# Optimization experiments

Measured on AMD Instinct MI355X. Metric: run time of the kernel, lower is better.

## Reference

```python
import jax, jax.numpy as jnp
import numpy as np

D_MODEL = 1024
NUM_HEADS = 16
D_K = D_MODEL // NUM_HEADS


def setup_inputs() -> dict:
    key = jax.random.key(0)
    ks = jax.random.split(key, 9)
    B, S = 4, 2048
    s = 1.0 / np.sqrt(D_MODEL)
    inp = {
        "x": jax.random.normal(ks[0], (B, S, D_MODEL), dtype=jnp.float32),
        "wq": jax.random.uniform(ks[1], (D_MODEL, D_MODEL), jnp.float32, -s, s),
        "bq": jax.random.uniform(ks[2], (D_MODEL,), jnp.float32, -s, s),
        "wk": jax.random.uniform(ks[3], (D_MODEL, D_MODEL), jnp.float32, -s, s),
        "bk": jax.random.uniform(ks[4], (D_MODEL,), jnp.float32, -s, s),
        "wv": jax.random.uniform(ks[5], (D_MODEL, D_MODEL), jnp.float32, -s, s),
        "bv": jax.random.uniform(ks[6], (D_MODEL,), jnp.float32, -s, s),
        "wo": jax.random.uniform(ks[7], (D_MODEL, D_MODEL), jnp.float32, -s, s),
        "bo": jax.random.uniform(ks[8], (D_MODEL,), jnp.float32, -s, s),
    }
    return inp


def reference(x, wq, bq, wk, bk, wv, bv, wo, bo):
    B, S, _ = x.shape
    H, Dk = NUM_HEADS, D_K
    # QKV projections; weights stored as (in, out) so y = x @ w + b
    q = (x @ wq + bq).reshape(B, S, H, Dk).transpose(0, 2, 1, 3)  # (B,H,S,Dk)
    k = (x @ wk + bk).reshape(B, S, H, Dk).transpose(0, 2, 1, 3)
    v = (x @ wv + bv).reshape(B, S, H, Dk).transpose(0, 2, 1, 3)
    scores = jnp.einsum("bhqd,bhkd->bhqk", q, k) / jnp.sqrt(jnp.float32(Dk))
    causal = jnp.tril(jnp.ones((S, S), dtype=bool))  # True = keep
    scores = jnp.where(causal, scores, jnp.float32(-jnp.inf))
    attn = jax.nn.softmax(scores, axis=-1)  # dropout=0 (eval)
    out = jnp.einsum("bhqk,bhkd->bhqd", attn, v)
    out = out.transpose(0, 2, 1, 3).reshape(B, S, H * Dk)
    return out @ wo + bo
```

## Files before the change

kernel.cpp:

```cpp
#include <hip/hip_runtime.h>
#include <hip/hip_bf16.h>


#define D_MODEL 1024
#define NHEADS  16
#define DK      64
#define BATCH   4
#define SEQ     2048
#define MROWS   (BATCH*SEQ)

typedef short bvec8 __attribute__((ext_vector_type(8)));
typedef float fvec4 __attribute__((ext_vector_type(4)));

__device__ __forceinline__ unsigned short f2bf(float f) {
    unsigned int x = __float_as_uint(f);
    x += 0x7fffu + ((x >> 16) & 1u);
    return (unsigned short)(x >> 16);
}

__device__ __forceinline__ unsigned pack_bf16x2(float a, float b) {
#if __has_builtin(__builtin_amdgcn_cvt_pk_bf16_f32)
    typedef __bf16 bf16x2_t __attribute__((ext_vector_type(2)));
    union { bf16x2_t v; unsigned u; } cv;
    cv.v = __builtin_amdgcn_cvt_pk_bf16_f32(a, b);
    return cv.u;
#else
    return (unsigned)f2bf(a) | ((unsigned)f2bf(b) << 16);
#endif
}

__device__ __forceinline__ float fast_exp2(float x) {
#if __has_builtin(__builtin_amdgcn_exp2f)
    return __builtin_amdgcn_exp2f(x);
#else
    return exp2f(x);
#endif
}


__global__ void f32_to_bf16_k(const float* __restrict__ in,
                              unsigned short* __restrict__ out, int n4) {
    int i = blockIdx.x * 256 + threadIdx.x;
    if (i < n4) {
        float4 v = ((const float4*)in)[i];
        ushort4 o;
        o.x = f2bf(v.x); o.y = f2bf(v.y); o.z = f2bf(v.z); o.w = f2bf(v.w);
        ((ushort4*)out)[i] = o;
    }
}

__global__ void transpose_to_bf16_k(const float* __restrict__ W,
                                    unsigned short* __restrict__ Wt) {
    __shared__ float tile[32][33];
    int n0 = blockIdx.x * 32, k0 = blockIdx.y * 32;
    int tx = threadIdx.x & 31;
    int ty = (threadIdx.x >> 5) * 4;
#pragma unroll
    for (int i = 0; i < 4; ++i)
        tile[ty + i][tx] = W[(k0 + ty + i) * D_MODEL + n0 + tx];
    __syncthreads();
#pragma unroll
    for (int i = 0; i < 4; ++i)
        Wt[(n0 + ty + i) * D_MODEL + k0 + tx] = f2bf(tile[tx][ty + i]);
}

__global__ void build_cbias_k(const float* __restrict__ bq, const float* __restrict__ bk,
                              const float* __restrict__ bv, float* __restrict__ cb) {
    int i = blockIdx.x * 256 + threadIdx.x;
    float v = (i < 1024) ? bq[i] : (i < 2048) ? bk[i - 1024] : bv[i - 2048];
    cb[i] = v;
}

__global__ __launch_bounds__(256, 4)
void gemm_glds(const unsigned short* __restrict__ A,
               const unsigned short* __restrict__ Bt,
               const float* __restrict__ bias,
               unsigned short* __restrict__ oq,
               unsigned short* __restrict__ ok,
               unsigned short* __restrict__ ov,
               float* __restrict__ of,
               float qscale, int mode) {
    __shared__ __align__(16) unsigned short As[128 * 64];
    __shared__ __align__(16) unsigned short Bs[128 * 64];

    const int tid  = threadIdx.x;
    const int lane = tid & 63;
    const int w    = tid >> 6;
    const int wr   = w >> 1, wc = w & 1;
    const int quad = lane >> 4, l16 = lane & 15;
    const int rowBlock = blockIdx.y * 128;
    const int colBlock = blockIdx.x * 128;

    const int lrow   = lane >> 3;
    const int gchunk = (lane & 7) ^ lrow;

    fvec4 acc[4][4] = {};

    for (int k0 = 0; k0 < D_MODEL; k0 += 64) {
        __syncthreads();
#pragma unroll
        for (int n = 0; n < 4; ++n) {
            const int g = w * 4 + n;
            const int ra = rowBlock + g * 8 + lrow;
            const int ca = colBlock + g * 8 + lrow;
            __builtin_amdgcn_global_load_lds(
                (const __attribute__((address_space(1))) void*)
                    &A[(size_t)ra * D_MODEL + k0 + gchunk * 8],
                (__attribute__((address_space(3))) void*)&As[g * 512], 16, 0, 0);
            __builtin_amdgcn_global_load_lds(
                (const __attribute__((address_space(1))) void*)
                    &Bt[(size_t)ca * D_MODEL + k0 + gchunk * 8],
                (__attribute__((address_space(3))) void*)&Bs[g * 512], 16, 0, 0);
        }
        __syncthreads();
#pragma unroll
        for (int kc = 0; kc < 2; ++kc) {
            bvec8 af[4], bfr[4];
#pragma unroll
            for (int i = 0; i < 4; ++i) {
                int r = wr * 64 + i * 16 + l16;
                af[i] = *(const bvec8*)&As[r * 64 + (((kc * 4 + quad) ^ (l16 & 7)) * 8)];
            }
#pragma unroll
            for (int j = 0; j < 4; ++j) {
                int r = wc * 64 + j * 16 + l16;
                bfr[j] = *(const bvec8*)&Bs[r * 64 + (((kc * 4 + quad) ^ (l16 & 7)) * 8)];
            }
#pragma unroll
            for (int i = 0; i < 4; ++i)
#pragma unroll
                for (int j = 0; j < 4; ++j)
                    acc[i][j] = __builtin_amdgcn_mfma_f32_16x16x32_bf16(
                        af[i], bfr[j], acc[i][j], 0, 0, 0);
        }
    }

    if (mode == 0) {
#pragma unroll
        for (int i = 0; i < 4; ++i) {
#pragma unroll
            for (int j = 0; j < 4; ++j) {
                int ncol = colBlock + wc * 64 + j * 16 + l16;
                int which = ncol >> 10;
                int nn = ncol & 1023;
                int h = nn >> 6, d = nn & 63;
                float bv = bias[ncol];
#pragma unroll
                for (int r = 0; r < 4; ++r) {
                    int mrow = rowBlock + wr * 64 + i * 16 + quad * 4 + r;
                    int b = mrow >> 11, s = mrow & (SEQ - 1);
                    float v = acc[i][j][r] + bv;
                    if (which == 0)
                        oq[(((b * NHEADS + h) * SEQ + s) * DK) + d] = f2bf(v * qscale);
                    else if (which == 1)
                        ok[(((b * NHEADS + h) * SEQ + s) * DK) + d] = f2bf(v);
                    else
                        ov[(((b * NHEADS + h) * DK + d) * SEQ) + s] = f2bf(v);
                }
            }
        }
    } else {
#pragma unroll
        for (int i = 0; i < 4; ++i) {
#pragma unroll
            for (int j = 0; j < 4; ++j) {
                int ncol = colBlock + wc * 64 + j * 16 + l16;
                float bv = bias[ncol];
#pragma unroll
                for (int r = 0; r < 4; ++r) {
                    int mrow = rowBlock + wr * 64 + i * 16 + quad * 4 + r;
                    of[(size_t)mrow * D_MODEL + ncol] = acc[i][j][r] + bv;
                }
            }
        }
    }
}

__global__ __launch_bounds__(256, 3)
void attn_mfma6(const unsigned short* __restrict__ Q,
                const unsigned short* __restrict__ K,
                const unsigned short* __restrict__ Vt,
                unsigned short* __restrict__ O) {
    __shared__ __align__(16) unsigned short Ksm[64 * 64];
    __shared__ __align__(16) unsigned short Vsm[64 * 64];
    __shared__ __align__(16) unsigned short Pl[4][32 * 64];

    const int tid  = threadIdx.x;
    const int lane = tid & 63;
    const int wq   = tid >> 6;
    const int quad = lane >> 4, l16 = lane & 15;
    const int bx = blockIdx.x;
    const int qt = (bx & 1) ? ((bx - 1) >> 1) : (15 - (bx >> 1));
    const int h = blockIdx.y, b = blockIdx.z;

    const size_t bhq = ((size_t)b * NHEADS + h) * SEQ * DK;
    const unsigned short* Qb = Q + bhq;
    const unsigned short* Kb = K + bhq;
    const unsigned short* Vb = Vt + bhq;

    const int q0 = qt * 128 + wq * 32;

    bvec8 qf[2][2];
#pragma unroll
    for (int qg = 0; qg < 2; ++qg)
#pragma unroll
        for (int kc = 0; kc < 2; ++kc)
            qf[qg][kc] = *(const bvec8*)&Qb[(q0 + qg * 16 + l16) * DK + kc * 32 + quad * 8];

    const int sr = tid >> 2;
    const int sc = tid & 3;
    const int sp0 = ((sc) ^ (sr & 7)) * 8;
    const int sp1 = ((sc + 4) ^ (sr & 7)) * 8;
    unsigned short* Pw = &Pl[wq][0];

    const int ktmax = 2 * qt + 1;
    const int ktact = 2 * qt + (wq >> 1);
    const int mofs  = (wq & 1) << 5;

    bvec8 kr0, kr1, vr0, vr1;
    {
        const unsigned short* kg = Kb + sr * DK;
        kr0 = *(const bvec8*)(kg + sc * 8);
        kr1 = *(const bvec8*)(kg + (sc + 4) * 8);
        const unsigned short* vg = Vb + sr * SEQ;
        vr0 = *(const bvec8*)(vg + sc * 8);
        vr1 = *(const bvec8*)(vg + (sc + 4) * 8);
    }

    fvec4 acc[2][4] = {};
    float lp[2] = {0.f, 0.f};

    for (int kt = 0; kt <= ktmax; ++kt) {
        *(bvec8*)&Ksm[sr * 64 + sp0] = kr0;
        *(bvec8*)&Ksm[sr * 64 + sp1] = kr1;
        *(bvec8*)&Vsm[sr * 64 + sp0] = vr0;
        *(bvec8*)&Vsm[sr * 64 + sp1] = vr1;
        __syncthreads();
        if (kt < ktmax) {
            const unsigned short* kg = Kb + ((kt + 1) * 64 + sr) * DK;
            kr0 = *(const bvec8*)(kg + sc * 8);
            kr1 = *(const bvec8*)(kg + (sc + 4) * 8);
            const unsigned short* vg = Vb + sr * SEQ + (kt + 1) * 64;
            vr0 = *(const bvec8*)(vg + sc * 8);
            vr1 = *(const bvec8*)(vg + (sc + 4) * 8);
        }
        if (kt <= ktact) {
#pragma unroll
            for (int t4 = 0; t4 < 4; ++t4) {
                fvec4 s[2] = {};
#pragma unroll
                for (int kc = 0; kc < 2; ++kc) {
                    bvec8 af = *(const bvec8*)
                        &Ksm[(t4 * 16 + l16) * 64 + (((kc * 4 + quad) ^ (l16 & 7)) * 8)];
#pragma unroll
                    for (int qg = 0; qg < 2; ++qg)
                        s[qg] = __builtin_amdgcn_mfma_f32_16x16x32_bf16(
                            af, qf[qg][kc], s[qg], 0, 0, 0);
                }
                if (kt == ktact) {
#pragma unroll
                    for (int qg = 0; qg < 2; ++qg)
#pragma unroll
                        for (int r = 0; r < 4; ++r) {
                            int key = t4 * 16 + quad * 4 + r - mofs;
                            int qq  = qg * 16 + l16;
                            if (key > qq) s[qg][r] = -__builtin_inff();
                        }
                }
#pragma unroll
                for (int qg = 0; qg < 2; ++qg) {
                    float p0 = fast_exp2(s[qg][0]);
                    float p1 = fast_exp2(s[qg][1]);
                    float p2 = fast_exp2(s[qg][2]);
                    float p3 = fast_exp2(s[qg][3]);
                    lp[qg] += (p0 + p1) + (p2 + p3);
                    uint2 pk;
                    pk.x = pack_bf16x2(p0, p1);
                    pk.y = pack_bf16x2(p2, p3);
                    *(uint2*)&Pw[(qg * 16 + l16) * 64 +
                                 (((t4 * 2 + (quad >> 1)) ^ (l16 & 7)) * 8) +
                                 (quad & 1) * 4] = pk;
                }
            }

#pragma unroll
            for (int kc = 0; kc < 2; ++kc) {
                bvec8 ap[2];
#pragma unroll
                for (int qg = 0; qg < 2; ++qg)
                    ap[qg] = *(const bvec8*)
                        &Pw[(qg * 16 + l16) * 64 + (((kc * 4 + quad) ^ (l16 & 7)) * 8)];
#pragma unroll
                for (int dt = 0; dt < 4; ++dt) {
                    bvec8 bv = *(const bvec8*)
                        &Vsm[(dt * 16 + l16) * 64 + (((kc * 4 + quad) ^ (l16 & 7)) * 8)];
#pragma unroll
                    for (int qg = 0; qg < 2; ++qg)
                        acc[qg][dt] = __builtin_amdgcn_mfma_f32_16x16x32_bf16(
                            ap[qg], bv, acc[qg][dt], 0, 0, 0);
                }
            }
        }
        __syncthreads();
    }

#pragma unroll
    for (int qg = 0; qg < 2; ++qg) {
        float lr = lp[qg];
        lr += __shfl_xor(lr, 16);
        lr += __shfl_xor(lr, 32);
        float invv[4];
#pragma unroll
        for (int r = 0; r < 4; ++r)
            invv[r] = 1.f / __shfl(lr, quad * 4 + r);
#pragma unroll
        for (int r = 0; r < 4; ++r) {
            size_t row = (size_t)(b * SEQ + q0 + qg * 16 + quad * 4 + r);
            unsigned short* dst = O + row * D_MODEL + h * DK + l16;
#pragma unroll
            for (int dt = 0; dt < 4; ++dt)
                dst[dt * 16] = f2bf(acc[qg][dt][r] * invv[r]);
        }
    }
}


extern "C" void kernel_launch(void* const* d_in, const int* in_sizes, int n_in,
                              void* d_out, int out_size, void* d_ws, size_t ws_size,
                              hipStream_t stream) {
    const float* x  = (const float*)d_in[0];
    const float* wq = (const float*)d_in[1];
    const float* bq = (const float*)d_in[2];
    const float* wk = (const float*)d_in[3];
    const float* bk = (const float*)d_in[4];
    const float* wv = (const float*)d_in[5];
    const float* bv = (const float*)d_in[6];
    const float* wo = (const float*)d_in[7];
    const float* bo = (const float*)d_in[8];
    float* out = (float*)d_out;

    char* ws = (char*)d_ws;
    const size_t MB = 1u << 20;
    unsigned short* xb    = (unsigned short*)(ws);
    unsigned short* wqkvt = (unsigned short*)(ws + 16 * MB);
    unsigned short* wot   = (unsigned short*)(ws + 22 * MB);
    unsigned short* qb    = (unsigned short*)(ws + 24 * MB);
    unsigned short* kb    = (unsigned short*)(ws + 40 * MB);
    unsigned short* vtb   = (unsigned short*)(ws + 56 * MB);
    unsigned short* ab    = (unsigned short*)(ws + 72 * MB);
    float* cbias = (float*)(ws + 72 * MB);

    f32_to_bf16_k<<<(MROWS * D_MODEL / 4 + 255) / 256, 256, 0, stream>>>(
        x, xb, MROWS * D_MODEL / 4);
    dim3 tg(32, 32);
    transpose_to_bf16_k<<<tg, 256, 0, stream>>>(wq, wqkvt);
    transpose_to_bf16_k<<<tg, 256, 0, stream>>>(wk, wqkvt + 1024 * 1024);
    transpose_to_bf16_k<<<tg, 256, 0, stream>>>(wv, wqkvt + 2 * 1024 * 1024);
    transpose_to_bf16_k<<<tg, 256, 0, stream>>>(wo, wot);
    build_cbias_k<<<12, 256, 0, stream>>>(bq, bk, bv, cbias);

    const float QSCALE = 0.125f * 1.44269504088896340736f;

    gemm_glds<<<dim3(3072 / 128, MROWS / 128), 256, 0, stream>>>(
        xb, wqkvt, cbias, qb, kb, vtb, nullptr, QSCALE, 0);

    attn_mfma6<<<dim3(SEQ / 128, NHEADS, BATCH), 256, 0, stream>>>(qb, kb, vtb, ab);

    gemm_glds<<<dim3(D_MODEL / 128, MROWS / 128), 256, 0, stream>>>(
        ab, wot, bo, nullptr, nullptr, nullptr, out, 1.0f, 1);
}
```

Measured before the change: 323.6 us.

## Double-buffer K/V tiles in attention, halve P scratch, merge weight transposes

The attention kernel now double-buffers the K and V shared-memory tiles. This removes the second barrier per key tile, since the next tile is written into the other buffer after compute. The P staging buffer is split into two 32-key halves interleaved with the PV MFMAs, which shrinks LDS use so launch bounds can target 4 blocks per CU. The four weight-transpose launches are merged into one kernel with a z grid dimension to cut launch overhead. The risk is higher register pressure at 4 waves per SIMD, plus the changed swizzle patterns.

After: 318.4 us. About the same (-1.6%).

```diff
diff --git a/kernel.cpp b/kernel.cpp
--- a/kernel.cpp
+++ b/kernel.cpp
@@ -49,9 +49,14 @@
     }
 }
 
-__global__ void transpose_to_bf16_k(const float* __restrict__ W,
-                                    unsigned short* __restrict__ Wt) {
+__global__ void transpose_all_k(const float* __restrict__ wq, const float* __restrict__ wk,
+                                const float* __restrict__ wv, const float* __restrict__ wo,
+                                unsigned short* __restrict__ wqkvt,
+                                unsigned short* __restrict__ wot) {
     __shared__ float tile[32][33];
+    const int z = blockIdx.z;
+    const float* W = (z == 0) ? wq : (z == 1) ? wk : (z == 2) ? wv : wo;
+    unsigned short* Wt = (z == 3) ? wot : wqkvt + (size_t)z * D_MODEL * D_MODEL;
     int n0 = blockIdx.x * 32, k0 = blockIdx.y * 32;
     int tx = threadIdx.x & 31;
     int ty = (threadIdx.x >> 5) * 4;
@@ -176,14 +181,14 @@
     }
 }
 
-__global__ __launch_bounds__(256, 3)
-void attn_mfma6(const unsigned short* __restrict__ Q,
+__global__ __launch_bounds__(256, 4)
+void attn_mfma7(const unsigned short* __restrict__ Q,
                 const unsigned short* __restrict__ K,
                 const unsigned short* __restrict__ Vt,
                 unsigned short* __restrict__ O) {
-    __shared__ __align__(16) unsigned short Ksm[64 * 64];
-    __shared__ __align__(16) unsigned short Vsm[64 * 64];
-    __shared__ __align__(16) unsigned short Pl[4][32 * 64];
+    __shared__ __align__(16) unsigned short Ksm[2][64 * 64];
+    __shared__ __align__(16) unsigned short Vsm[2][64 * 64];
+    __shared__ __align__(16) unsigned short Pl[4][32 * 32];
 
     const int tid  = threadIdx.x;
     const int lane = tid & 63;
@@ -225,17 +230,18 @@
         const unsigned short* vg = Vb + sr * SEQ;
         vr0 = *(const bvec8*)(vg + sc * 8);
         vr1 = *(const bvec8*)(vg + (sc + 4) * 8);
+        *(bvec8*)&Ksm[0][sr * 64 + sp0] = kr0;
+        *(bvec8*)&Ksm[0][sr * 64 + sp1] = kr1;
+        *(bvec8*)&Vsm[0][sr * 64 + sp0] = vr0;
+        *(bvec8*)&Vsm[0][sr * 64 + sp1] = vr1;
     }
 
     fvec4 acc[2][4] = {};
     float lp[2] = {0.f, 0.f};
 
     for (int kt = 0; kt <= ktmax; ++kt) {
-        *(bvec8*)&Ksm[sr * 64 + sp0] = kr0;
-        *(bvec8*)&Ksm[sr * 64 + sp1] = kr1;
-        *(bvec8*)&Vsm[sr * 64 + sp0] = vr0;
-        *(bvec8*)&Vsm[sr * 64 + sp1] = vr1;
         __syncthreads();
+        const int buf = kt & 1;
         if (kt < ktmax) {
             const unsigned short* kg = Kb + ((kt + 1) * 64 + sr) * DK;
             kr0 = *(const bvec8*)(kg + sc * 8);
@@ -245,55 +251,57 @@
             vr1 = *(const bvec8*)(vg + (sc + 4) * 8);
         }
         if (kt <= ktact) {
-#pragma unroll
-            for (int t4 = 0; t4 < 4; ++t4) {
-                fvec4 s[2] = {};
-#pragma unroll
-                for (int kc = 0; kc < 2; ++kc) {
-                    bvec8 af = *(const bvec8*)
-                        &Ksm[(t4 * 16 + l16) * 64 + (((kc * 4 + quad) ^ (l16 & 7)) * 8)];
-#pragma unroll
-                    for (int qg = 0; qg < 2; ++qg)
-                        s[qg] = __builtin_amdgcn_mfma_f32_16x16x32_bf16(
-                            af, qf[qg][kc], s[qg], 0, 0, 0);
+            const unsigned short* Kbuf = &Ksm[buf][0];
+            const unsigned short* Vbuf = &Vsm[buf][0];
+#pragma unroll
+            for (int half = 0; half < 2; ++half) {
+#pragma unroll
+                for (int tl = 0; tl < 2; ++tl) {
+                    const int t4 = half * 2 + tl;
+                    fvec4 s[2] = {};
+#pragma unroll
+                    for (int kc = 0; kc < 2; ++kc) {
+                        bvec8 af = *(const bvec8*)
+                            &Kbuf[(t4 * 16 + l16) * 64 + (((kc * 4 + quad) ^ (l16 & 7)) * 8)];
+#pragma unroll
+                        for (int qg = 0; qg < 2; ++qg)
+                            s[qg] = __builtin_amdgcn_mfma_f32_16x16x32_bf16(
+                                af, qf[qg][kc], s[qg], 0, 0, 0);
+                    }
+                    if (kt == ktact) {
+#pragma unroll
+                        for (int qg = 0; qg < 2; ++qg)
+#pragma unroll
+                            for (int r = 0; r < 4; ++r) {
+                                int key = t4 * 16 + quad * 4 + r - mofs;
+                                int qq  = qg * 16 + l16;
+                                if (key > qq) s[qg][r] = -__builtin_inff();
+                            }
+                    }
+#pragma unroll
+                    for (int qg = 0; qg < 2; ++qg) {
+                        float p0 = fast_exp2(s[qg][0]);
+                        float p1 = fast_exp2(s[qg][1]);
+                        float p2 = fast_exp2(s[qg][2]);
+                        float p3 = fast_exp2(s[qg][3]);
+                        lp[qg] += (p0 + p1) + (p2 + p3);
+                        uint2 pk;
+                        pk.x = pack_bf16x2(p0, p1);
+                        pk.y = pack_bf16x2(p2, p3);
+                        *(uint2*)&Pw[(qg * 16 + l16) * 32 +
+                                     (((tl * 2 + (quad >> 1)) ^ (l16 & 3)) * 8) +
+                                     (quad & 1) * 4] = pk;
+                    }
                 }
-                if (kt == ktact) {
-#pragma unroll
-                    for (int qg = 0; qg < 2; ++qg)
-#pragma unroll
-                        for (int r = 0; r < 4; ++r) {
-                            int key = t4 * 16 + quad * 4 + r - mofs;
-                            int qq  = qg * 16 + l16;
-                            if (key > qq) s[qg][r] = -__builtin_inff();
-                        }
-                }
-#pragma unroll
-                for (int qg = 0; qg < 2; ++qg) {
-                    float p0 = fast_exp2(s[qg][0]);
-                    float p1 = fast_exp2(s[qg][1]);
-                    float p2 = fast_exp2(s[qg][2]);
-                    float p3 = fast_exp2(s[qg][3]);
-                    lp[qg] += (p0 + p1) + (p2 + p3);
-                    uint2 pk;
-                    pk.x = pack_bf16x2(p0, p1);
-                    pk.y = pack_bf16x2(p2, p3);
-                    *(uint2*)&Pw[(qg * 16 + l16) * 64 +
-                                 (((t4 * 2 + (quad >> 1)) ^ (l16 & 7)) * 8) +
-                                 (quad & 1) * 4] = pk;
-                }
-            }
-
-#pragma unroll
-            for (int kc = 0; kc < 2; ++kc) {
                 bvec8 ap[2];
 #pragma unroll
                 for (int qg = 0; qg < 2; ++qg)
                     ap[qg] = *(const bvec8*)
-                        &Pw[(qg * 16 + l16) * 64 + (((kc * 4 + quad) ^ (l16 & 7)) * 8)];
+                        &Pw[(qg * 16 + l16) * 32 + ((quad ^ (l16 & 3)) * 8)];
 #pragma unroll
                 for (int dt = 0; dt < 4; ++dt) {
                     bvec8 bv = *(const bvec8*)
-                        &Vsm[(dt * 16 + l16) * 64 + (((kc * 4 + quad) ^ (l16 & 7)) * 8)];
+                        &Vbuf[(dt * 16 + l16) * 64 + (((half * 4 + quad) ^ (l16 & 7)) * 8)];
 #pragma unroll
                     for (int qg = 0; qg < 2; ++qg)
                         acc[qg][dt] = __builtin_amdgcn_mfma_f32_16x16x32_bf16(
@@ -301,7 +309,13 @@
                 }
             }
         }
-        __syncthreads();
+        if (kt < ktmax) {
+            const int nb = buf ^ 1;
+            *(bvec8*)&Ksm[nb][sr * 64 + sp0] = kr0;
+            *(bvec8*)&Ksm[nb][sr * 64 + sp1] = kr1;
+            *(bvec8*)&Vsm[nb][sr * 64 + sp0] = vr0;
+            *(bvec8*)&Vsm[nb][sr * 64 + sp1] = vr1;
+        }
     }
 
 #pragma unroll
@@ -352,11 +366,7 @@
 
     f32_to_bf16_k<<<(MROWS * D_MODEL / 4 + 255) / 256, 256, 0, stream>>>(
         x, xb, MROWS * D_MODEL / 4);
-    dim3 tg(32, 32);
-    transpose_to_bf16_k<<<tg, 256, 0, stream>>>(wq, wqkvt);
-    transpose_to_bf16_k<<<tg, 256, 0, stream>>>(wk, wqkvt + 1024 * 1024);
-    transpose_to_bf16_k<<<tg, 256, 0, stream>>>(wv, wqkvt + 2 * 1024 * 1024);
-    transpose_to_bf16_k<<<tg, 256, 0, stream>>>(wo, wot);
+    transpose_all_k<<<dim3(32, 32, 4), 256, 0, stream>>>(wq, wk, wv, wo, wqkvt, wot);
     build_cbias_k<<<12, 256, 0, stream>>>(bq, bk, bv, cbias);
 
     const float QSCALE = 0.125f * 1.44269504088896340736f;
@@ -364,7 +374,7 @@
     gemm_glds<<<dim3(3072 / 128, MROWS / 128), 256, 0, stream>>>(
         xb, wqkvt, cbias, qb, kb, vtb, nullptr, QSCALE, 0);
 
-    attn_mfma6<<<dim3(SEQ / 128, NHEADS, BATCH), 256, 0, stream>>>(qb, kb, vtb, ab);
+    attn_mfma7<<<dim3(SEQ / 128, NHEADS, BATCH), 256, 0, stream>>>(qb, kb, vtb, ab);
 
     gemm_glds<<<dim3(D_MODEL / 128, MROWS / 128), 256, 0, stream>>>(
         ab, wot, bo, nullptr, nullptr, nullptr, out, 1.0f, 1);
```
